# Kernel tuning notes

Hardware: AMD Instinct MI355X
Metric: run time of the kernel (lower is better)

## Reference

```python
import jax, jax.numpy as jnp
import numpy as np

NUM_EMBEDDINGS = 1024
EMBEDDING_DIM = 128
COMMITMENT_COEF = 0.25
DECAY = 0.99
EPS = 1e-5


def setup_inputs() -> dict:
    key = jax.random.key(0)
    k1, k2 = jax.random.split(key)
    z_e = jax.random.normal(k1, (64, EMBEDDING_DIM, 32, 32), dtype=jnp.float32)
    lim = 1.0 / NUM_EMBEDDINGS
    embed = jax.random.uniform(k2, (NUM_EMBEDDINGS, EMBEDDING_DIM), dtype=jnp.float32,
                               minval=-lim, maxval=lim)
    ema_cluster_size = jnp.zeros((NUM_EMBEDDINGS,), dtype=jnp.float32)
    ema_w = embed.copy()  # buffer initialized as clone of embed weights
    return {"z_e": z_e, "embed": embed,
            "ema_cluster_size": ema_cluster_size, "ema_w": ema_w}


def reference(z_e, embed, ema_cluster_size, ema_w):
    B, D, H, W = z_e.shape
    K = embed.shape[0]
    # [B,D,H,W] -> [N,D]
    flat = jnp.transpose(z_e, (0, 2, 3, 1)).reshape(-1, D)
    distances = (jnp.sum(flat ** 2, axis=1, keepdims=True)
                 + jnp.sum(embed ** 2, axis=1)
                 - 2.0 * jnp.matmul(flat, embed.T))
    encoding_indices = jnp.argmin(distances, axis=1)  # [N]

    quantized = embed[encoding_indices].reshape(B, H, W, D)
    quantized = jnp.transpose(quantized, (0, 3, 1, 2))  # [B,D,H,W]

    # ---- EMA codebook update (training path) ----
    N = flat.shape[0]
    cluster_size = jax.ops.segment_sum(jnp.ones((N,), flat.dtype),
                                       encoding_indices, num_segments=K)
    new_ema_cluster_size = DECAY * ema_cluster_size + (1.0 - DECAY) * cluster_size
    dw = jax.ops.segment_sum(flat, encoding_indices, num_segments=K)  # encodings^T @ flat
    new_ema_w = DECAY * ema_w + (1.0 - DECAY) * dw
    n = jnp.sum(new_ema_cluster_size)
    cs = (new_ema_cluster_size + EPS) / (n + K * EPS) * n
    new_embed = new_ema_w / cs[:, None]

    commitment_loss = jnp.mean((jax.lax.stop_gradient(quantized) - z_e) ** 2)
    loss = commitment_loss * COMMITMENT_COEF
    # straight-through estimator
    quantized_st = z_e + jax.lax.stop_gradient(quantized - z_e)
    indices = encoding_indices.reshape(B, H * W)
    return (quantized_st, indices, loss, new_embed, new_ema_cluster_size, new_ema_w)
```

## Files before the change

### kernel.cpp

```cpp
#include <hip/hip_runtime.h>

#define K_CODES 1024
#define DIM 128
#define HW 1024
#define NTOT 65536
#define DECAY 0.99f
#define OMD 0.01f
#define EPS 1e-5f
#define CCOEF 0.25f
#define MARGIN 1e-4f
#define FLCAP 24576

#define OFF_Q    0
#define OFF_IDX  8388608
#define OFF_LOSS (8388608 + 65536)
#define OFF_EMB  (OFF_LOSS + 1)
#define OFF_ECS  (OFF_EMB + 131072)
#define OFF_EMAW (OFF_ECS + 1024)

#define W_NORM2 0
#define W_RCP   1024
#define W_HIST  2048
#define W_LOSS  3072
#define W_FLCNT 3073
#define W_CNT2  3076
#define W_FL    (3076 + 24576)
#define W_M1F   (27652 + 24576)
#define W_CAND  (52228 + 24576)
#define W_EH    (76804 + 196608)
#define W_EL    (273412 + 65536)
#define W_NXIDX (338948 + 65536)
#define W_FLAT  (404484 + 65536)
#define W_NEED  (470020 + 8388608)

typedef __attribute__((ext_vector_type(8))) short short8v;
typedef __attribute__((ext_vector_type(4))) float f32x4;

__device__ __forceinline__ unsigned short f2bf(float f) {
    unsigned u = __float_as_uint(f);
    u += 0x7fffu + ((u >> 16) & 1u);
    return (unsigned short)(u >> 16);
}
__device__ __forceinline__ float bf2f(unsigned short h) {
    return __uint_as_float(((unsigned)h) << 16);
}

__global__ __launch_bounds__(256) void kzero(float* __restrict__ p, int n) {
    int i = blockIdx.x * 256 + threadIdx.x;
    if (i < n) p[i] = 0.f;
}

__device__ __forceinline__ float np_pairwise_sumsq_128(const float* p, size_t stride) {
    float r[8][4];
    #pragma unroll
    for (int j = 0; j < 8; ++j)
        #pragma unroll
        for (int L = 0; L < 4; ++L) {
            float x = p[(size_t)(j * 4 + L) * stride];
            r[j][L] = __fmul_rn(x, x);
        }
    #pragma unroll
    for (int c = 1; c < 4; ++c)
        #pragma unroll
        for (int j = 0; j < 8; ++j)
            #pragma unroll
            for (int L = 0; L < 4; ++L) {
                float x = p[(size_t)(c * 32 + j * 4 + L) * stride];
                r[j][L] = __fadd_rn(r[j][L], __fmul_rn(x, x));
            }
    float V[4];
    #pragma unroll
    for (int L = 0; L < 4; ++L) {
        float a = __fadd_rn(r[0][L], r[1][L]);
        float b = __fadd_rn(r[2][L], r[3][L]);
        float c2 = __fadd_rn(r[4][L], r[5][L]);
        float d2 = __fadd_rn(r[6][L], r[7][L]);
        V[L] = __fadd_rn(__fadd_rn(a, b), __fadd_rn(c2, d2));
    }
    return __fadd_rn(__fadd_rn(V[0], V[1]), __fadd_rn(V[2], V[3]));
}

__global__ __launch_bounds__(256) void kpre(
    const float* __restrict__ ze, float* __restrict__ nx,
    float* __restrict__ flat_c, const float* __restrict__ embed,
    float* __restrict__ norm2, unsigned short* __restrict__ ehs_g,
    unsigned short* __restrict__ els_g, float* __restrict__ zero_p, int zero_n)
{
    __shared__ float t[128][133];
    const int tid = threadIdx.x;
    const int bid = blockIdx.x;
    if (bid < 512) {
        const int n0 = bid * 128;
        const int b = n0 >> 10, hw0 = n0 & (HW - 1);
        const float* zb = ze + (size_t)b * (DIM * HW) + hw0;
        #pragma unroll
        for (int i = 0; i < 64; ++i) {
            int d = i * 2 + (tid >> 7);
            int hw = tid & 127;
            t[hw][d] = zb[(size_t)d * HW + hw];
        }
        __syncthreads();
        if (tid < 128) nx[n0 + tid] = np_pairwise_sumsq_128(&t[tid][0], 1);
        if (flat_c) {
            #pragma unroll
            for (int i = 0; i < 16; ++i) {
                int lin = i * 256 + tid;
                int r  = lin >> 5;
                int c4 = lin & 31;
                float4 v = *(const float4*)&t[r][c4 * 4];
                *(float4*)&flat_c[(size_t)(n0 + r) * DIM + c4 * 4] = v;
            }
        }
    } else {
        const int pid = bid - 512;
        int zi = pid * 256 + tid;
        if (zi < zero_n) zero_p[zi] = 0.f;
        {
            const int g32 = tid >> 5, l32 = tid & 31;
            const int k = pid * 8 + g32;
            const float* row = embed + (size_t)k * DIM;
            float x = row[l32];
            float r = __fmul_rn(x, x);
            #pragma unroll
            for (int c = 1; c < 4; ++c) {
                float y = row[c * 32 + l32];
                r = __fadd_rn(r, __fmul_rn(y, y));
            }
            float s1 = __fadd_rn(r, __shfl_xor(r, 4, 64));
            float s2 = __fadd_rn(s1, __shfl_xor(s1, 8, 64));
            float s3 = __fadd_rn(s2, __shfl_xor(s2, 16, 64));
            float h1 = __fadd_rn(s3, __shfl_xor(s3, 1, 64));
            float h2 = __fadd_rn(h1, __shfl_xor(h1, 2, 64));
            if (l32 == 0) norm2[k] = h2;
        }
        if (ehs_g) {
            int hu = pid * 256 + tid;
            int U = hu >> 1, half = hu & 1;
            int code = U >> 4;
            int g = (U & 15) ^ (code & 15);
            const float* src = embed + (size_t)code * DIM + g * 8 + half * 4;
            float4 f = *(const float4*)src;
            unsigned short a = f2bf(f.x), b = f2bf(f.y), c = f2bf(f.z), d = f2bf(f.w);
            ushort4 hi; hi.x = a; hi.y = b; hi.z = c; hi.w = d;
            ushort4 lo;
            lo.x = f2bf(f.x - bf2f(a)); lo.y = f2bf(f.y - bf2f(b));
            lo.z = f2bf(f.z - bf2f(c)); lo.w = f2bf(f.w - bf2f(d));
            *(ushort4*)(ehs_g + (size_t)U * 8 + half * 4) = hi;
            *(ushort4*)(els_g + (size_t)U * 8 + half * 4) = lo;
        }
    }
}

__global__ __launch_bounds__(256, 4) void kapprox(
    const float* __restrict__ flat_c, const unsigned short* __restrict__ eh_g,
    const unsigned short* __restrict__ el_g, const float* __restrict__ norm2,
    int* __restrict__ idx_ws, float* __restrict__ idx_out,
    unsigned* __restrict__ hist, unsigned* __restrict__ flcnt,
    unsigned* __restrict__ fl_list, float* __restrict__ m1f)
{
    __shared__ __align__(16) unsigned short ehs[2][32 * 128];
    __shared__ __align__(16) unsigned short els[2][32 * 128];
    __shared__ float nes[1024];

    const int tid = threadIdx.x;
    const int l = tid & 63;
    const int w = tid >> 6;
    const int lg = l >> 4;
    const int lm = l & 15;
    const int n0 = blockIdx.x * 64;

    for (int i = tid; i < 1024; i += 256) nes[i] = norm2[i];

    short8v xh[4], xl[4];
    {
        const float* xr = flat_c + (size_t)(n0 + w * 16 + lm) * DIM;
        #pragma unroll
        for (int ks = 0; ks < 4; ++ks) {
            int kb = ks * 32 + lg * 8;
            float f0[8];
            *(float4*)&f0[0] = *(const float4*)(xr + kb);
            *(float4*)&f0[4] = *(const float4*)(xr + kb + 4);
            #pragma unroll
            for (int e = 0; e < 8; ++e) {
                unsigned short h0 = f2bf(f0[e]);
                xh[ks][e] = (short)h0;
                xl[ks][e] = (short)f2bf(f0[e] - bf2f(h0));
            }
        }
    }

    int roff[4];
    #pragma unroll
    for (int ks = 0; ks < 4; ++ks)
        roff[ks] = lm * 128 + (((ks * 4 + lg) ^ lm) * 8);

    const int su0 = tid * 8;
    const int su1 = 2048 + tid * 8;

    uint4 peh0 = *(const uint4*)(eh_g + su0);
    uint4 peh1 = *(const uint4*)(eh_g + su1);
    uint4 pel0 = *(const uint4*)(el_g + su0);
    uint4 pel1 = *(const uint4*)(el_g + su1);
    *(uint4*)&ehs[0][su0] = peh0;
    *(uint4*)&ehs[0][su1] = peh1;
    *(uint4*)&els[0][su0] = pel0;
    *(uint4*)&els[0][su1] = pel1;
    __syncthreads();

    float m1 = 3.4e38f, m2 = 3.4e38f;
    int c1 = 0;

    for (int it = 0; it < 32; ++it) {
        const int buf = it & 1;
        const int nt = it + 1;
        if (nt < 32) {
            const size_t nb = (size_t)nt * 4096;
            peh0 = *(const uint4*)(eh_g + nb + su0);
            peh1 = *(const uint4*)(eh_g + nb + su1);
            pel0 = *(const uint4*)(el_g + nb + su0);
            pel1 = *(const uint4*)(el_g + nb + su1);
        }
        f32x4 a00 = {0.f,0.f,0.f,0.f}, a01 = {0.f,0.f,0.f,0.f};
        const unsigned short* be = &ehs[buf][0];
        const unsigned short* bl = &els[buf][0];
        #pragma unroll
        for (int ks = 0; ks < 4; ++ks) {
            short8v eA = *(const short8v*)(be + roff[ks]);
            short8v lA = *(const short8v*)(bl + roff[ks]);
            short8v eB = *(const short8v*)(be + 2048 + roff[ks]);
            short8v lB = *(const short8v*)(bl + 2048 + roff[ks]);
            a00 = __builtin_amdgcn_mfma_f32_16x16x32_bf16(eA, xh[ks], a00, 0, 0, 0);
            a00 = __builtin_amdgcn_mfma_f32_16x16x32_bf16(lA, xh[ks], a00, 0, 0, 0);
            a00 = __builtin_amdgcn_mfma_f32_16x16x32_bf16(eA, xl[ks], a00, 0, 0, 0);
            a01 = __builtin_amdgcn_mfma_f32_16x16x32_bf16(eB, xh[ks], a01, 0, 0, 0);
            a01 = __builtin_amdgcn_mfma_f32_16x16x32_bf16(lB, xh[ks], a01, 0, 0, 0);
            a01 = __builtin_amdgcn_mfma_f32_16x16x32_bf16(eB, xl[ks], a01, 0, 0, 0);
        }
        #pragma unroll
        for (int r = 0; r < 4; ++r) {
            int code0 = it * 32 + lg * 4 + r;
            int code1 = code0 + 16;
            float s0 = nes[code0] - 2.f * a00[r];
            float s1 = nes[code1] - 2.f * a01[r];
            m2 = fminf(m2, fmaxf(m1, s0));
            if (s0 < m1) { m1 = s0; c1 = code0; }
            m2 = fminf(m2, fmaxf(m1, s1));
            if (s1 < m1) { m1 = s1; c1 = code1; }
        }
        if (nt < 32) {
            *(uint4*)&ehs[buf ^ 1][su0] = peh0;
            *(uint4*)&ehs[buf ^ 1][su1] = peh1;
            *(uint4*)&els[buf ^ 1][su0] = pel0;
            *(uint4*)&els[buf ^ 1][su1] = pel1;
        }
        __syncthreads();
    }

    #pragma unroll
    for (int mk = 16; mk <= 32; mk <<= 1) {
        float om1 = __shfl_xor(m1, mk, 64);
        int   oc1 = __shfl_xor(c1, mk, 64);
        float om2 = __shfl_xor(m2, mk, 64);
        m2 = fminf(fminf(m2, om2), fmaxf(m1, om1));
        if (om1 < m1 || (om1 == m1 && oc1 < c1)) { m1 = om1; c1 = oc1; }
    }
    if (lg == 0) {
        int n = n0 + w * 16 + lm;
        if (m2 - m1 > MARGIN) {
            idx_ws[n] = c1;
            idx_out[n] = (float)c1;
            atomicAdd(&hist[c1], 1u);
        } else {
            unsigned p = atomicAdd(flcnt, 1u);
            if (p < FLCAP) { fl_list[p] = (unsigned)n; m1f[p] = m1; }
            else {
                idx_ws[n] = c1; idx_out[n] = (float)c1;
                atomicAdd(&hist[c1], 1u);
            }
        }
    }
}

__global__ __launch_bounds__(256, 2) void kapprox2(
    const float* __restrict__ flat_c, const unsigned short* __restrict__ eh_g,
    const unsigned short* __restrict__ el_g, const float* __restrict__ norm2,
    const float* __restrict__ m1f, const unsigned* __restrict__ flcnt,
    const unsigned* __restrict__ fl_list, unsigned* __restrict__ cnt_g,
    unsigned* __restrict__ cand_g)
{
    __shared__ __align__(16) unsigned short ehs[2][32 * 128];
    __shared__ __align__(16) unsigned short els[2][32 * 128];
    __shared__ float nes[1024];
    __shared__ unsigned ccnt[128];
    __shared__ unsigned ccode[128][8];
    __shared__ int rid[128];
    __shared__ float thrs[128];

    const int tid = threadIdx.x;
    const int l = tid & 63;
    const int w = tid >> 6;
    const int lg = l >> 4;
    const int lm = l & 15;

    for (int i = tid; i < 1024; i += 256) nes[i] = norm2[i];

    int roff[4];
    #pragma unroll
    for (int ks = 0; ks < 4; ++ks)
        roff[ks] = lm * 128 + (((ks * 4 + lg) ^ lm) * 8);

    const int su0 = tid * 8;
    const int su1 = 2048 + tid * 8;

    unsigned nflag = flcnt[0];
    if (nflag > FLCAP) nflag = FLCAP;
    const unsigned nbat = (nflag + 127u) >> 7;
    const unsigned nwork = nbat * 8u;

    for (unsigned wi = blockIdx.x; wi < nwork; wi += gridDim.x) {
        const unsigned bat = wi >> 3;
        const int cq = (int)(wi & 7u);
        __syncthreads();
        if (tid < 128) {
            unsigned p = bat * 128u + tid;
            int n = (p < nflag) ? (int)fl_list[p] : -1;
            rid[tid] = n;
            thrs[tid] = (n >= 0) ? m1f[p] + MARGIN : -3.4e38f;
            ccnt[tid] = 0;
        }
        __syncthreads();

        const int lr0 = w * 32 + lm, lr1 = lr0 + 16;
        const int nr0 = rid[lr0], nr1 = rid[lr1];
        const float thr0 = thrs[lr0], thr1 = thrs[lr1];
        short8v xh0[4], xl0[4], xh1[4], xl1[4];
        {
            const float* xr0 = flat_c + (size_t)(nr0 < 0 ? 0 : nr0) * DIM;
            const float* xr1 = flat_c + (size_t)(nr1 < 0 ? 0 : nr1) * DIM;
            #pragma unroll
            for (int ks = 0; ks < 4; ++ks) {
                int kb = ks * 32 + lg * 8;
                float f0[8], f1[8];
                *(float4*)&f0[0] = *(const float4*)(xr0 + kb);
                *(float4*)&f0[4] = *(const float4*)(xr0 + kb + 4);
                *(float4*)&f1[0] = *(const float4*)(xr1 + kb);
                *(float4*)&f1[4] = *(const float4*)(xr1 + kb + 4);
                #pragma unroll
                for (int e = 0; e < 8; ++e) {
                    unsigned short h0 = f2bf(f0[e]);
                    unsigned short h1 = f2bf(f1[e]);
                    xh0[ks][e] = (short)h0;
                    xl0[ks][e] = (short)f2bf(f0[e] - bf2f(h0));
                    xh1[ks][e] = (short)h1;
                    xl1[ks][e] = (short)f2bf(f1[e] - bf2f(h1));
                }
            }
        }

        const int it0 = cq * 4;
        uint4 peh0, peh1, pel0, pel1;
        {
            const size_t nb = (size_t)it0 * 4096;
            peh0 = *(const uint4*)(eh_g + nb + su0);
            peh1 = *(const uint4*)(eh_g + nb + su1);
            pel0 = *(const uint4*)(el_g + nb + su0);
            pel1 = *(const uint4*)(el_g + nb + su1);
            *(uint4*)&ehs[0][su0] = peh0;
            *(uint4*)&ehs[0][su1] = peh1;
            *(uint4*)&els[0][su0] = pel0;
            *(uint4*)&els[0][su1] = pel1;
        }
        __syncthreads();

        for (int ii = 0; ii < 4; ++ii) {
            const int it = it0 + ii;
            const int buf = ii & 1;
            if (ii + 1 < 4) {
                const size_t nb = (size_t)(it + 1) * 4096;
                peh0 = *(const uint4*)(eh_g + nb + su0);
                peh1 = *(const uint4*)(eh_g + nb + su1);
                pel0 = *(const uint4*)(el_g + nb + su0);
                pel1 = *(const uint4*)(el_g + nb + su1);
            }
            f32x4 a00 = {0.f,0.f,0.f,0.f}, a01 = {0.f,0.f,0.f,0.f};
            f32x4 a10 = {0.f,0.f,0.f,0.f}, a11 = {0.f,0.f,0.f,0.f};
            const unsigned short* be = &ehs[buf][0];
            const unsigned short* bl = &els[buf][0];
            #pragma unroll
            for (int ks = 0; ks < 4; ++ks) {
                short8v eA = *(const short8v*)(be + roff[ks]);
                short8v lA = *(const short8v*)(bl + roff[ks]);
                short8v eB = *(const short8v*)(be + 2048 + roff[ks]);
                short8v lB = *(const short8v*)(bl + 2048 + roff[ks]);
                a00 = __builtin_amdgcn_mfma_f32_16x16x32_bf16(eA, xh0[ks], a00, 0, 0, 0);
                a00 = __builtin_amdgcn_mfma_f32_16x16x32_bf16(lA, xh0[ks], a00, 0, 0, 0);
                a00 = __builtin_amdgcn_mfma_f32_16x16x32_bf16(eA, xl0[ks], a00, 0, 0, 0);
                a10 = __builtin_amdgcn_mfma_f32_16x16x32_bf16(eA, xh1[ks], a10, 0, 0, 0);
                a10 = __builtin_amdgcn_mfma_f32_16x16x32_bf16(lA, xh1[ks], a10, 0, 0, 0);
                a10 = __builtin_amdgcn_mfma_f32_16x16x32_bf16(eA, xl1[ks], a10, 0, 0, 0);
                a01 = __builtin_amdgcn_mfma_f32_16x16x32_bf16(eB, xh0[ks], a01, 0, 0, 0);
                a01 = __builtin_amdgcn_mfma_f32_16x16x32_bf16(lB, xh0[ks], a01, 0, 0, 0);
                a01 = __builtin_amdgcn_mfma_f32_16x16x32_bf16(eB, xl0[ks], a01, 0, 0, 0);
                a11 = __builtin_amdgcn_mfma_f32_16x16x32_bf16(eB, xh1[ks], a11, 0, 0, 0);
                a11 = __builtin_amdgcn_mfma_f32_16x16x32_bf16(lB, xh1[ks], a11, 0, 0, 0);
                a11 = __builtin_amdgcn_mfma_f32_16x16x32_bf16(eB, xl1[ks], a11, 0, 0, 0);
            }
            #pragma unroll
            for (int r = 0; r < 4; ++r) {
                int code0 = it * 32 + lg * 4 + r;
                int code1 = code0 + 16;
                float s00 = nes[code0] - 2.f * a00[r];
                float s01 = nes[code1] - 2.f * a01[r];
                float s10 = nes[code0] - 2.f * a10[r];
                float s11 = nes[code1] - 2.f * a11[r];
                if (s00 <= thr0) {
                    unsigned p = atomicAdd(&ccnt[lr0], 1u);
                    if (p < 8) ccode[lr0][p] = (unsigned)code0;
                }
                if (s01 <= thr0) {
                    unsigned p = atomicAdd(&ccnt[lr0], 1u);
                    if (p < 8) ccode[lr0][p] = (unsigned)code1;
                }
                if (s10 <= thr1) {
                    unsigned p = atomicAdd(&ccnt[lr1], 1u);
                    if (p < 8) ccode[lr1][p] = (unsigned)code0;
                }
                if (s11 <= thr1) {
                    unsigned p = atomicAdd(&ccnt[lr1], 1u);
                    if (p < 8) ccode[lr1][p] = (unsigned)code1;
                }
            }
            if (ii + 1 < 4) {
                *(uint4*)&ehs[buf ^ 1][su0] = peh0;
                *(uint4*)&ehs[buf ^ 1][su1] = peh1;
                *(uint4*)&els[buf ^ 1][su0] = pel0;
                *(uint4*)&els[buf ^ 1][su1] = pel1;
            }
            __syncthreads();
        }

        if (tid < 128) {
            int n = rid[tid];
            unsigned lc = ccnt[tid];
            if (lc > 8u) lc = 8u;
            if (n >= 0 && lc > 0) {
                unsigned p = bat * 128u + tid;
                unsigned base = atomicAdd(&cnt_g[p], lc);
                for (unsigned j = 0; j < lc; ++j) {
                    unsigned slot = base + j;
                    if (slot < 8u) cand_g[(size_t)p * 8 + slot] = ccode[tid][j];
                }
            }
        }
    }
}

__global__ __launch_bounds__(256) void krescore(
    const float* __restrict__ flat_c, const float* __restrict__ embed,
    const float* __restrict__ norm2, const float* nxg,
    const unsigned* __restrict__ flcnt, const unsigned* __restrict__ fl_list,
    const unsigned* __restrict__ cnt_g, const unsigned* __restrict__ cand_g,
    int* idx_ws, float* __restrict__ idx_out, unsigned* __restrict__ hist)
{
    unsigned nflag = flcnt[0];
    if (nflag > FLCAP) nflag = FLCAP;
    for (unsigned p = blockIdx.x * 256u + threadIdx.x; p < nflag;
         p += gridDim.x * 256u) {
        const int n = (int)fl_list[p];
        unsigned c = cnt_g[p];
        if (c > 8u) c = 8u;
        unsigned cc[8];
        uint4 pk0 = *(const uint4*)(cand_g + (size_t)p * 8);
        uint4 pk1 = *(const uint4*)(cand_g + (size_t)p * 8 + 4);
        cc[0] = pk0.x; cc[1] = pk0.y; cc[2] = pk0.z; cc[3] = pk0.w;
        cc[4] = pk1.x; cc[5] = pk1.y; cc[6] = pk1.z; cc[7] = pk1.w;
        int bestk = (int)cc[0];
        if (c > 1) {
            float bests = 3.4e38f;
            bestk = 1 << 30;
            const float* xr = flat_c + (size_t)n * DIM;
            const float nx = nxg[n];
            #pragma unroll
            for (int q = 0; q < 8; ++q) {
                if (q < (int)c) {
                    int k = (int)cc[q];
                    const float* er = embed + (size_t)k * DIM;
                    float dot = 0.f;
                    #pragma unroll
                    for (int d4 = 0; d4 < 32; ++d4) {
                        float4 e4 = *(const float4*)(er + d4 * 4);
                        float4 x4 = *(const float4*)(xr + d4 * 4);
                        dot = fmaf(x4.x, e4.x, dot);
                        dot = fmaf(x4.y, e4.y, dot);
                        dot = fmaf(x4.z, e4.z, dot);
                        dot = fmaf(x4.w, e4.w, dot);
                    }
                    float qv = __fadd_rn(nx, norm2[k]);
                    float s = __fsub_rn(qv, __fmul_rn(2.f, dot));
                    if (s < bests || (s == bests && k < bestk)) { bests = s; bestk = k; }
                }
            }
        }
        idx_ws[n] = bestk;
        idx_out[n] = (float)bestk;
        atomicAdd(&hist[bestk], 1u);
    }
}

__global__ __launch_bounds__(256) void kfin_r(
    const unsigned int* __restrict__ hist, const float* __restrict__ ema_cs,
    float* __restrict__ out_ecs, float* __restrict__ rcp)
{
    const int tid = threadIdx.x;
    __shared__ float wsum[4];
    float local = 0.f;
    float necs[4];
    #pragma unroll
    for (int u = 0; u < 4; ++u) {
        int k = u * 256 + tid;
        necs[u] = DECAY * ema_cs[k] + OMD * (float)hist[k];
        out_ecs[k] = necs[u];
        local += necs[u];
    }
    #pragma unroll
    for (int off = 32; off >= 1; off >>= 1) local += __shfl_xor(local, off, 64);
    if ((tid & 63) == 0) wsum[tid >> 6] = local;
    __syncthreads();
    float ntot = wsum[0] + wsum[1] + wsum[2] + wsum[3];
    #pragma unroll
    for (int u = 0; u < 4; ++u) {
        int k = u * 256 + tid;
        float cs = (necs[u] + EPS) / (ntot + (float)K_CODES * EPS) * ntot;
        rcp[k] = 1.f / cs;
    }
}

__global__ __launch_bounds__(64) void kloss(
    float* __restrict__ loss_out, const float* __restrict__ loss_acc)
{
    if (threadIdx.x == 0)
        loss_out[0] = loss_acc[0] * (CCOEF / (float)((size_t)NTOT * DIM));
}

__global__ __launch_bounds__(512) void ktail(
    const float* __restrict__ ze, const float* __restrict__ embed,
    const int* __restrict__ idx_ws, float* __restrict__ qout,
    float* __restrict__ loss_acc, const float* __restrict__ flat_c,
    const float* __restrict__ ema_w, const float* __restrict__ rcp,
    float* __restrict__ out_emb, float* __restrict__ out_emaw)
{
    __shared__ float shmem[64 * 133];
    __shared__ int idxs[64];
    __shared__ float lsum[8];
    const int tid = threadIdx.x;
    const int bid = blockIdx.x;
    if (bid < 1024) {
        const int n0 = bid * 64;
        const int b = n0 >> 10;
        const int hw0 = n0 & (HW - 1);
        if (tid < 64) idxs[tid] = idx_ws[n0 + tid];
        __syncthreads();
        #pragma unroll
        for (int it = 0; it < 4; ++it) {
            int lin = it * 512 + tid;
            int r = lin >> 5, c4 = lin & 31;
            float4 v = *(const float4*)(embed + (size_t)idxs[r] * DIM + c4 * 4);
            *(float4*)&shmem[r * 133 + c4 * 4] = v;
        }
        __syncthreads();
        const float* zb = ze + (size_t)b * (DIM * HW) + hw0;
        float* qb = qout + (size_t)b * (DIM * HW) + hw0;
        const int hwl = tid & 63;
        float lacc = 0.f;
        #pragma unroll 4
        for (int dd = 0; dd < 16; ++dd) {
            int d = dd * 8 + (tid >> 6);
            float val = shmem[hwl * 133 + d];
            size_t off = (size_t)d * HW + hwl;
            float z = zb[off];
            qb[off] = val;
            float diff = val - z;
            lacc = fmaf(diff, diff, lacc);
        }
        #pragma unroll
        for (int off = 32; off >= 1; off >>= 1) lacc += __shfl_xor(lacc, off, 64);
        if ((tid & 63) == 0) lsum[tid >> 6] = lacc;
        __syncthreads();
        if (tid == 0) {
            float s = ((lsum[0] + lsum[1]) + (lsum[2] + lsum[3]))
                    + ((lsum[4] + lsum[5]) + (lsum[6] + lsum[7]));
            atomicAdd(loss_acc, s);
        }
    } else {
        float (*part)[128] = (float(*)[128])shmem;
        const int k = bid - 1024;
        const int lane = tid & 63;
        const int w = tid >> 6;
        float lo = 0.f, hi = 0.f;
        const int nbeg = w * (NTOT / 8);
        const int nend = nbeg + (NTOT / 8);
        for (int base = nbeg; base < nend; base += 64) {
            int my = idx_ws[base + lane];
            unsigned long long m = __ballot(my == k);
            while (m) {
                int bit = __ffsll((long long)m) - 1;
                m &= m - 1;
                const float* row = flat_c + (size_t)(base + bit) * DIM;
                lo += row[lane];
                hi += row[lane + 64];
            }
        }
        part[w][lane] = lo;
        part[w][lane + 64] = hi;
        __syncthreads();
        if (w == 0) {
            float a = part[0][lane], bsum = part[0][lane + 64];
            #pragma unroll
            for (int u = 1; u < 8; ++u) {
                a += part[u][lane];
                bsum += part[u][lane + 64];
            }
            const float r = rcp[k];
            int elo = k * DIM + lane, ehi = elo + 64;
            float nwa = DECAY * ema_w[elo] + OMD * a;
            float nwb = DECAY * ema_w[ehi] + OMD * bsum;
            out_emaw[elo] = nwa;
            out_emaw[ehi] = nwb;
            out_emb[elo] = nwa * r;
            out_emb[ehi] = nwb * r;
        }
    }
}

__global__ __launch_bounds__(256, 2) void kargmin(
    const float* __restrict__ ze, const float* __restrict__ embed,
    const float* __restrict__ norm2, const float* nxg,
    int* idx_ws, float* __restrict__ idx_out,
    unsigned int* __restrict__ hist)
{
    __shared__ float xs[128 * 36];
    __shared__ float es[128 * 36];
    __shared__ float nxs[128];
    const int tid = threadIdx.x;
    const int tx = tid & 15, ty = tid >> 4;
    const int n0 = blockIdx.x * 128;
    const float* zbase = ze + (size_t)(n0 >> 10) * (DIM * HW) + (n0 & (HW - 1));
    if (tid < 128) nxs[tid] = nxg[n0 + tid];
    float minv[8];
    int   mini[8];
    #pragma unroll
    for (int i = 0; i < 8; ++i) { minv[i] = 3.4e38f; mini[i] = 0; }
    for (int kt = 0; kt < 8; ++kt) {
        float acc[8][8];
        #pragma unroll
        for (int i = 0; i < 8; ++i)
            #pragma unroll
            for (int j = 0; j < 8; ++j) acc[i][j] = 0.f;
        for (int dc = 0; dc < 4; ++dc) {
            __syncthreads();
            #pragma unroll
            for (int it = 0; it < 4; ++it) {
                int lin = it * 256 + tid;
                int r  = lin & 127;
                int gu = lin >> 7;
                const float* gp = zbase + (size_t)(dc * 32 + gu * 4) * HW + r;
                float4 v;
                v.x = gp[0]; v.y = gp[HW]; v.z = gp[2 * HW]; v.w = gp[3 * HW];
                *(float4*)&xs[r * 36 + gu * 4] = v;
            }
            #pragma unroll
            for (int it = 0; it < 4; ++it) {
                int lin = it * 256 + tid;
                int k  = lin >> 3;
                int gu = lin & 7;
                float4 v = *(const float4*)(embed + (size_t)(kt * 128 + k) * DIM + dc * 32 + gu * 4);
                *(float4*)&es[k * 36 + gu * 4] = v;
            }
            __syncthreads();
            #pragma unroll
            for (int g = 0; g < 8; ++g) {
                float4 xf[8];
                #pragma unroll
                for (int i = 0; i < 8; ++i)
                    xf[i] = *(const float4*)&xs[(ty + i * 16) * 36 + g * 4];
                #pragma unroll
                for (int j = 0; j < 8; ++j) {
                    float4 ef = *(const float4*)&es[(tx + j * 16) * 36 + g * 4];
                    #pragma unroll
                    for (int i = 0; i < 8; ++i) {
                        acc[i][j] = fmaf(xf[i].x, ef.x, acc[i][j]);
                        acc[i][j] = fmaf(xf[i].y, ef.y, acc[i][j]);
                        acc[i][j] = fmaf(xf[i].z, ef.z, acc[i][j]);
                        acc[i][j] = fmaf(xf[i].w, ef.w, acc[i][j]);
                    }
                }
            }
        }
        #pragma unroll
        for (int j = 0; j < 8; ++j) {
            int kg = kt * 128 + tx + j * 16;
            float nrm = norm2[kg];
            #pragma unroll
            for (int i = 0; i < 8; ++i) {
                float q = __fadd_rn(nxs[ty + i * 16], nrm);
                float t = __fmul_rn(2.f, acc[i][j]);
                float s = __fsub_rn(q, t);
                if (s < minv[i]) { minv[i] = s; mini[i] = kg; }
            }
        }
    }
    #pragma unroll
    for (int i = 0; i < 8; ++i) {
        float v = minv[i]; int ix = mini[i];
        #pragma unroll
        for (int off = 8; off >= 1; off >>= 1) {
            float v2 = __shfl_xor(v, off, 16);
            int   i2 = __shfl_xor(ix, off, 16);
            if (v2 < v || (v2 == v && i2 < ix)) { v = v2; ix = i2; }
        }
        if (tx == 0) {
            int n = n0 + ty + i * 16;
            idx_ws[n] = ix;
            idx_out[n] = (float)ix;
            atomicAdd(&hist[ix], 1u);
        }
    }
}

__global__ __launch_bounds__(256) void kquant(
    const float* __restrict__ ze, const float* __restrict__ embed,
    const int* __restrict__ idx_ws, float* __restrict__ qout,
    float* __restrict__ dw_atomic, float* __restrict__ loss_acc)
{
    __shared__ float q[128 * 133];
    __shared__ int idxs[128];
    __shared__ float lsum[4];
    const int tid = threadIdx.x;
    const int n0 = blockIdx.x * 128;
    const int b = n0 >> 10;
    const int hw0 = n0 & (HW - 1);
    if (tid < 128) idxs[tid] = idx_ws[n0 + tid];
    __syncthreads();
    #pragma unroll
    for (int it = 0; it < 16; ++it) {
        int r = it * 8 + (tid >> 5);
        int c = tid & 31;
        float4 v = *(const float4*)(embed + (size_t)idxs[r] * DIM + c * 4);
        *(float4*)&q[r * 133 + c * 4] = v;
    }
    __syncthreads();
    const float* zb = ze + (size_t)b * (DIM * HW) + hw0;
    float* qb = qout + (size_t)b * (DIM * HW) + hw0;
    float lacc = 0.f;
    for (int dd = 0; dd < 64; ++dd) {
        int d = dd * 2 + (tid >> 7);
        int hw = tid & 127;
        float val = q[hw * 133 + d];
        size_t off = (size_t)d * HW + hw;
        float z = zb[off];
        qb[off] = val;
        float diff = val - z;
        lacc = fmaf(diff, diff, lacc);
        if (dw_atomic) atomicAdd(&dw_atomic[idxs[hw] * DIM + d], z);
    }
    #pragma unroll
    for (int off = 32; off >= 1; off >>= 1) lacc += __shfl_xor(lacc, off, 64);
    if ((tid & 63) == 0) lsum[tid >> 6] = lacc;
    __syncthreads();
    if (tid == 0) atomicAdd(loss_acc, lsum[0] + lsum[1] + lsum[2] + lsum[3]);
}

__global__ __launch_bounds__(256) void kfin1(
    const unsigned int* __restrict__ hist, const float* __restrict__ ema_cs,
    float* __restrict__ out_ecs, float* __restrict__ rcp,
    float* __restrict__ loss_out, const float* __restrict__ loss_acc)
{
    const int tid = threadIdx.x;
    __shared__ float wsum[4];
    float local = 0.f;
    float necs[4];
    #pragma unroll
    for (int u = 0; u < 4; ++u) {
        int k = u * 256 + tid;
        necs[u] = DECAY * ema_cs[k] + OMD * (float)hist[k];
        out_ecs[k] = necs[u];
        local += necs[u];
    }
    #pragma unroll
    for (int off = 32; off >= 1; off >>= 1) local += __shfl_xor(local, off, 64);
    if ((tid & 63) == 0) wsum[tid >> 6] = local;
    __syncthreads();
    float ntot = wsum[0] + wsum[1] + wsum[2] + wsum[3];
    #pragma unroll
    for (int u = 0; u < 4; ++u) {
        int k = u * 256 + tid;
        float cs = (necs[u] + EPS) / (ntot + (float)K_CODES * EPS) * ntot;
        rcp[k] = 1.f / cs;
    }
    if (tid == 0) loss_out[0] = loss_acc[0] * (CCOEF / (float)((size_t)NTOT * DIM));
}

__global__ __launch_bounds__(256) void kfin2(
    const float* __restrict__ ema_w, const float* __restrict__ dw,
    const float* __restrict__ rcp, float* __restrict__ out_emb,
    float* __restrict__ out_emaw)
{
    int e = blockIdx.x * 256 + threadIdx.x;
    int k = e >> 7;
    float nw = DECAY * ema_w[e] + OMD * dw[e];
    out_emaw[e] = nw;
    out_emb[e] = nw * rcp[k];
}

extern "C" void kernel_launch(void* const* d_in, const int* in_sizes, int n_in,
                              void* d_out, int out_size, void* d_ws, size_t ws_size,
                              hipStream_t stream) {
    const float* ze     = (const float*)d_in[0];
    const float* embed  = (const float*)d_in[1];
    const float* ema_cs = (const float*)d_in[2];
    const float* ema_w  = (const float*)d_in[3];
    float* out = (float*)d_out;

    float* ws = (float*)d_ws;
    float*          ws_norm2 = ws + W_NORM2;
    float*          ws_rcp   = ws + W_RCP;
    unsigned*       ws_hist  = (unsigned*)(ws + W_HIST);
    float*          ws_loss  = ws + W_LOSS;
    unsigned*       ws_flcnt = (unsigned*)(ws + W_FLCNT);
    unsigned*       ws_cnt   = (unsigned*)(ws + W_CNT2);
    unsigned*       ws_fl    = (unsigned*)(ws + W_FL);
    float*          ws_m1    = ws + W_M1F;
    unsigned*       ws_cand  = (unsigned*)(ws + W_CAND);
    float*          ws_dw    = ws + W_CAND;
    unsigned short* ws_eh    = (unsigned short*)(ws + W_EH);
    unsigned short* ws_el    = (unsigned short*)(ws + W_EL);
    float*          ws_nx    = ws + W_NXIDX;
    int*            ws_idx   = (int*)(ws + W_NXIDX);
    float*          ws_flat  = ws + W_FLAT;
    const size_t need = (size_t)W_NEED * sizeof(float);
    const bool big_ws = ws_size >= need;

    if (big_ws) {
        hipLaunchKernelGGL(kpre, dim3(640), dim3(256), 0, stream,
                           ze, ws_nx, ws_flat, embed, ws_norm2, ws_eh, ws_el,
                           (float*)ws_hist, 25604);
        hipLaunchKernelGGL(kapprox, dim3(1024), dim3(256), 0, stream,
                           ws_flat, ws_eh, ws_el, ws_norm2,
                           ws_idx, out + OFF_IDX, ws_hist, ws_flcnt, ws_fl, ws_m1);
        hipLaunchKernelGGL(kapprox2, dim3(512), dim3(256), 0, stream,
                           ws_flat, ws_eh, ws_el, ws_norm2,
                           ws_m1, ws_flcnt, ws_fl, ws_cnt, ws_cand);
        hipLaunchKernelGGL(krescore, dim3(64), dim3(256), 0, stream,
                           ws_flat, embed, ws_norm2, ws_nx, ws_flcnt, ws_fl,
                           ws_cnt, ws_cand, ws_idx, out + OFF_IDX, ws_hist);
        hipLaunchKernelGGL(kfin_r, dim3(1), dim3(256), 0, stream,
                           ws_hist, ema_cs, out + OFF_ECS, ws_rcp);
        hipLaunchKernelGGL(ktail, dim3(2048), dim3(512), 0, stream,
                           ze, embed, ws_idx, out + OFF_Q, ws_loss,
                           ws_flat, ema_w, ws_rcp, out + OFF_EMB, out + OFF_EMAW);
        hipLaunchKernelGGL(kloss, dim3(1), dim3(64), 0, stream,
                           out + OFF_LOSS, ws_loss);
    } else {
        hipLaunchKernelGGL(kpre, dim3(640), dim3(256), 0, stream,
                           ze, ws_nx, (float*)nullptr, embed, ws_norm2,
                           (unsigned short*)nullptr, (unsigned short*)nullptr,
                           (float*)ws_hist, 1028);
        hipLaunchKernelGGL(kzero, dim3(512), dim3(256), 0, stream, ws_dw, 131072);
        hipLaunchKernelGGL(kargmin, dim3(512), dim3(256), 0, stream,
                           ze, embed, ws_norm2, ws_nx, ws_idx, out + OFF_IDX, ws_hist);
        hipLaunchKernelGGL(kquant, dim3(512), dim3(256), 0, stream,
                           ze, embed, ws_idx, out + OFF_Q, ws_dw, ws_loss);
        hipLaunchKernelGGL(kfin1, dim3(1), dim3(256), 0, stream,
                           ws_hist, ema_cs, out + OFF_ECS, ws_rcp, out + OFF_LOSS, ws_loss);
        hipLaunchKernelGGL(kfin2, dim3(512), dim3(256), 0, stream,
                           ema_w, ws_dw, ws_rcp, out + OFF_EMB, out + OFF_EMAW);
    }
}
```

Measured before the change: 170.3 us.

## Fold finalize and loss kernels into predecessors via last-block atomic counters

```diff
diff --git a/kernel.cpp b/kernel.cpp
--- a/kernel.cpp
+++ b/kernel.cpp
@@ -23,6 +23,8 @@
 #define W_HIST  2048
 #define W_LOSS  3072
 #define W_FLCNT 3073
+#define W_RDONE 3074
+#define W_QDONE 3075
 #define W_CNT2  3076
 #define W_FL    (3076 + 24576)
 #define W_M1F   (27652 + 24576)
@@ -207,8 +209,8 @@
     *(uint4*)&els[0][su1] = pel1;
     __syncthreads();
 
-    float m1 = 3.4e38f, m2 = 3.4e38f;
-    int c1 = 0;
+    float m1a = 3.4e38f, m2a = 3.4e38f, m1b = 3.4e38f, m2b = 3.4e38f;
+    int c1a = 0, c1b = 0;
 
     for (int it = 0; it < 32; ++it) {
         const int buf = it & 1;
@@ -242,10 +244,10 @@
             int code1 = code0 + 16;
             float s0 = nes[code0] - 2.f * a00[r];
             float s1 = nes[code1] - 2.f * a01[r];
-            m2 = fminf(m2, fmaxf(m1, s0));
-            if (s0 < m1) { m1 = s0; c1 = code0; }
-            m2 = fminf(m2, fmaxf(m1, s1));
-            if (s1 < m1) { m1 = s1; c1 = code1; }
+            m2a = fminf(m2a, fmaxf(m1a, s0));
+            if (s0 < m1a) { m1a = s0; c1a = code0; }
+            m2b = fminf(m2b, fmaxf(m1b, s1));
+            if (s1 < m1b) { m1b = s1; c1b = code1; }
         }
         if (nt < 32) {
             *(uint4*)&ehs[buf ^ 1][su0] = peh0;
@@ -255,6 +257,10 @@
         }
         __syncthreads();
     }
+
+    float m1 = m1a, m2 = fminf(fminf(m2a, m2b), fmaxf(m1a, m1b));
+    int c1 = c1a;
+    if (m1b < m1a || (m1b == m1a && c1b < c1a)) { m1 = m1b; c1 = c1b; }
 
     #pragma unroll
     for (int mk = 16; mk <= 32; mk <<= 1) {
@@ -460,7 +466,9 @@
     const float* __restrict__ norm2, const float* nxg,
     const unsigned* __restrict__ flcnt, const unsigned* __restrict__ fl_list,
     const unsigned* __restrict__ cnt_g, const unsigned* __restrict__ cand_g,
-    int* idx_ws, float* __restrict__ idx_out, unsigned* __restrict__ hist)
+    int* idx_ws, float* __restrict__ idx_out, unsigned* hist,
+    unsigned* __restrict__ rdone, const float* __restrict__ ema_cs,
+    float* __restrict__ out_ecs, float* __restrict__ rcp)
 {
     unsigned nflag = flcnt[0];
     if (nflag > FLCAP) nflag = FLCAP;
@@ -505,49 +513,44 @@
         idx_out[n] = (float)bestk;
         atomicAdd(&hist[bestk], 1u);
     }
-}
-
-__global__ __launch_bounds__(256) void kfin_r(
-    const unsigned int* __restrict__ hist, const float* __restrict__ ema_cs,
-    float* __restrict__ out_ecs, float* __restrict__ rcp)
-{
-    const int tid = threadIdx.x;
-    __shared__ float wsum[4];
-    float local = 0.f;
-    float necs[4];
-    #pragma unroll
-    for (int u = 0; u < 4; ++u) {
-        int k = u * 256 + tid;
-        necs[u] = DECAY * ema_cs[k] + OMD * (float)hist[k];
-        out_ecs[k] = necs[u];
-        local += necs[u];
-    }
-    #pragma unroll
-    for (int off = 32; off >= 1; off >>= 1) local += __shfl_xor(local, off, 64);
-    if ((tid & 63) == 0) wsum[tid >> 6] = local;
+    __shared__ unsigned lastv;
+    __threadfence();
+    if (threadIdx.x == 0) lastv = atomicAdd(rdone, 1u);
     __syncthreads();
-    float ntot = wsum[0] + wsum[1] + wsum[2] + wsum[3];
-    #pragma unroll
-    for (int u = 0; u < 4; ++u) {
-        int k = u * 256 + tid;
-        float cs = (necs[u] + EPS) / (ntot + (float)K_CODES * EPS) * ntot;
-        rcp[k] = 1.f / cs;
-    }
-}
-
-__global__ __launch_bounds__(64) void kloss(
-    float* __restrict__ loss_out, const float* __restrict__ loss_acc)
-{
-    if (threadIdx.x == 0)
-        loss_out[0] = loss_acc[0] * (CCOEF / (float)((size_t)NTOT * DIM));
+    if (lastv == gridDim.x - 1) {
+        const int tid = threadIdx.x;
+        __shared__ float wsum[4];
+        float local = 0.f;
+        float necs[4];
+        #pragma unroll
+        for (int u = 0; u < 4; ++u) {
+            int k = u * 256 + tid;
+            unsigned h = atomicAdd(&hist[k], 0u);
+            necs[u] = DECAY * ema_cs[k] + OMD * (float)h;
+            out_ecs[k] = necs[u];
+            local += necs[u];
+        }
+        #pragma unroll
+        for (int off = 32; off >= 1; off >>= 1) local += __shfl_xor(local, off, 64);
+        if ((tid & 63) == 0) wsum[tid >> 6] = local;
+        __syncthreads();
+        float ntot = wsum[0] + wsum[1] + wsum[2] + wsum[3];
+        #pragma unroll
+        for (int u = 0; u < 4; ++u) {
+            int k = u * 256 + tid;
+            float cs = (necs[u] + EPS) / (ntot + (float)K_CODES * EPS) * ntot;
+            rcp[k] = 1.f / cs;
+        }
+    }
 }
 
 __global__ __launch_bounds__(512) void ktail(
     const float* __restrict__ ze, const float* __restrict__ embed,
     const int* __restrict__ idx_ws, float* __restrict__ qout,
-    float* __restrict__ loss_acc, const float* __restrict__ flat_c,
+    float* loss_acc, const float* __restrict__ flat_c,
     const float* __restrict__ ema_w, const float* __restrict__ rcp,
-    float* __restrict__ out_emb, float* __restrict__ out_emaw)
+    float* __restrict__ out_emb, float* __restrict__ out_emaw,
+    unsigned* __restrict__ qdone, float* __restrict__ loss_out)
 {
     __shared__ float shmem[64 * 133];
     __shared__ int idxs[64];
@@ -590,6 +593,12 @@
             float s = ((lsum[0] + lsum[1]) + (lsum[2] + lsum[3]))
                     + ((lsum[4] + lsum[5]) + (lsum[6] + lsum[7]));
             atomicAdd(loss_acc, s);
+            __threadfence();
+            unsigned old = atomicAdd(qdone, 1u);
+            if (old == 1023u) {
+                float tot = atomicAdd(loss_acc, 0.f);
+                loss_out[0] = tot * (CCOEF / (float)((size_t)NTOT * DIM));
+            }
         }
     } else {
         float (*part)[128] = (float(*)[128])shmem;
@@ -827,6 +836,8 @@
     unsigned*       ws_hist  = (unsigned*)(ws + W_HIST);
     float*          ws_loss  = ws + W_LOSS;
     unsigned*       ws_flcnt = (unsigned*)(ws + W_FLCNT);
+    unsigned*       ws_rdone = (unsigned*)(ws + W_RDONE);
+    unsigned*       ws_qdone = (unsigned*)(ws + W_QDONE);
     unsigned*       ws_cnt   = (unsigned*)(ws + W_CNT2);
     unsigned*       ws_fl    = (unsigned*)(ws + W_FL);
     float*          ws_m1    = ws + W_M1F;
@@ -852,14 +863,12 @@
                            ws_m1, ws_flcnt, ws_fl, ws_cnt, ws_cand);
         hipLaunchKernelGGL(krescore, dim3(64), dim3(256), 0, stream,
                            ws_flat, embed, ws_norm2, ws_nx, ws_flcnt, ws_fl,
-                           ws_cnt, ws_cand, ws_idx, out + OFF_IDX, ws_hist);
-        hipLaunchKernelGGL(kfin_r, dim3(1), dim3(256), 0, stream,
-                           ws_hist, ema_cs, out + OFF_ECS, ws_rcp);
+                           ws_cnt, ws_cand, ws_idx, out + OFF_IDX, ws_hist,
+                           ws_rdone, ema_cs, out + OFF_ECS, ws_rcp);
         hipLaunchKernelGGL(ktail, dim3(2048), dim3(512), 0, stream,
                            ze, embed, ws_idx, out + OFF_Q, ws_loss,
-                           ws_flat, ema_w, ws_rcp, out + OFF_EMB, out + OFF_EMAW);
-        hipLaunchKernelGGL(kloss, dim3(1), dim3(64), 0, stream,
-                           out + OFF_LOSS, ws_loss);
+                           ws_flat, ema_w, ws_rcp, out + OFF_EMB, out + OFF_EMAW,
+                           ws_qdone, out + OFF_LOSS);
     } else {
         hipLaunchKernelGGL(kpre, dim3(640), dim3(256), 0, stream,
                            ze, ws_nx, (float*)nullptr, embed, ws_norm2,
```

Measured after the change: 200.8 us. 1.18x slower.

## Switch kapprox to 32x32x16 MFMA with 32 rows per wave

Applied to the files above, without the earlier changes.

```diff
diff --git a/kernel.cpp b/kernel.cpp
--- a/kernel.cpp
+++ b/kernel.cpp
@@ -35,6 +35,7 @@
 
 typedef __attribute__((ext_vector_type(8))) short short8v;
 typedef __attribute__((ext_vector_type(4))) float f32x4;
+typedef __attribute__((ext_vector_type(16))) float f32x16;
 
 __device__ __forceinline__ unsigned short f2bf(float f) {
     unsigned u = __float_as_uint(f);
@@ -151,7 +152,7 @@
     }
 }
 
-__global__ __launch_bounds__(256, 4) void kapprox(
+__global__ __launch_bounds__(256, 2) void kapprox(
     const float* __restrict__ flat_c, const unsigned short* __restrict__ eh_g,
     const unsigned short* __restrict__ el_g, const float* __restrict__ norm2,
     int* __restrict__ idx_ws, float* __restrict__ idx_out,
@@ -165,18 +166,18 @@
     const int tid = threadIdx.x;
     const int l = tid & 63;
     const int w = tid >> 6;
-    const int lg = l >> 4;
-    const int lm = l & 15;
-    const int n0 = blockIdx.x * 64;
+    const int hi = l >> 5;
+    const int ln = l & 31;
+    const int n0 = blockIdx.x * 128;
 
     for (int i = tid; i < 1024; i += 256) nes[i] = norm2[i];
 
-    short8v xh[4], xl[4];
+    short8v xh[8], xl[8];
     {
-        const float* xr = flat_c + (size_t)(n0 + w * 16 + lm) * DIM;
-        #pragma unroll
-        for (int ks = 0; ks < 4; ++ks) {
-            int kb = ks * 32 + lg * 8;
+        const float* xr = flat_c + (size_t)(n0 + w * 32 + ln) * DIM;
+        #pragma unroll
+        for (int ks = 0; ks < 8; ++ks) {
+            int kb = ks * 16 + hi * 8;
             float f0[8];
             *(float4*)&f0[0] = *(const float4*)(xr + kb);
             *(float4*)&f0[4] = *(const float4*)(xr + kb + 4);
@@ -189,10 +190,10 @@
         }
     }
 
-    int roff[4];
-    #pragma unroll
-    for (int ks = 0; ks < 4; ++ks)
-        roff[ks] = lm * 128 + (((ks * 4 + lg) ^ lm) * 8);
+    int roff[8];
+    #pragma unroll
+    for (int ks = 0; ks < 8; ++ks)
+        roff[ks] = ln * 128 + ((((ks * 2) + hi) ^ (l & 15)) * 8);
 
     const int su0 = tid * 8;
     const int su1 = 2048 + tid * 8;
@@ -220,32 +221,26 @@
             pel0 = *(const uint4*)(el_g + nb + su0);
             pel1 = *(const uint4*)(el_g + nb + su1);
         }
-        f32x4 a00 = {0.f,0.f,0.f,0.f}, a01 = {0.f,0.f,0.f,0.f};
+        f32x16 accA = {0.f,0.f,0.f,0.f,0.f,0.f,0.f,0.f,
+                       0.f,0.f,0.f,0.f,0.f,0.f,0.f,0.f};
+        f32x16 accB = accA;
         const unsigned short* be = &ehs[buf][0];
         const unsigned short* bl = &els[buf][0];
         #pragma unroll
-        for (int ks = 0; ks < 4; ++ks) {
-            short8v eA = *(const short8v*)(be + roff[ks]);
-            short8v lA = *(const short8v*)(bl + roff[ks]);
-            short8v eB = *(const short8v*)(be + 2048 + roff[ks]);
-            short8v lB = *(const short8v*)(bl + 2048 + roff[ks]);
-            a00 = __builtin_amdgcn_mfma_f32_16x16x32_bf16(eA, xh[ks], a00, 0, 0, 0);
-            a00 = __builtin_amdgcn_mfma_f32_16x16x32_bf16(lA, xh[ks], a00, 0, 0, 0);
-            a00 = __builtin_amdgcn_mfma_f32_16x16x32_bf16(eA, xl[ks], a00, 0, 0, 0);
-            a01 = __builtin_amdgcn_mfma_f32_16x16x32_bf16(eB, xh[ks], a01, 0, 0, 0);
-            a01 = __builtin_amdgcn_mfma_f32_16x16x32_bf16(lB, xh[ks], a01, 0, 0, 0);
-            a01 = __builtin_amdgcn_mfma_f32_16x16x32_bf16(eB, xl[ks], a01, 0, 0, 0);
-        }
-        #pragma unroll
-        for (int r = 0; r < 4; ++r) {
-            int code0 = it * 32 + lg * 4 + r;
-            int code1 = code0 + 16;
-            float s0 = nes[code0] - 2.f * a00[r];
-            float s1 = nes[code1] - 2.f * a01[r];
-            m2 = fminf(m2, fmaxf(m1, s0));
-            if (s0 < m1) { m1 = s0; c1 = code0; }
-            m2 = fminf(m2, fmaxf(m1, s1));
-            if (s1 < m1) { m1 = s1; c1 = code1; }
+        for (int ks = 0; ks < 8; ++ks) {
+            short8v eh8 = *(const short8v*)(be + roff[ks]);
+            short8v el8 = *(const short8v*)(bl + roff[ks]);
+            accA = __builtin_amdgcn_mfma_f32_32x32x16_bf16(eh8, xh[ks], accA, 0, 0, 0);
+            accA = __builtin_amdgcn_mfma_f32_32x32x16_bf16(el8, xh[ks], accA, 0, 0, 0);
+            accB = __builtin_amdgcn_mfma_f32_32x32x16_bf16(eh8, xl[ks], accB, 0, 0, 0);
+        }
+        #pragma unroll
+        for (int r = 0; r < 16; ++r) {
+            int code = it * 32 + (r & 3) + 8 * (r >> 2) + 4 * hi;
+            float a = accA[r] + accB[r];
+            float s = nes[code] - 2.f * a;
+            m2 = fminf(m2, fmaxf(m1, s));
+            if (s < m1) { m1 = s; c1 = code; }
         }
         if (nt < 32) {
             *(uint4*)&ehs[buf ^ 1][su0] = peh0;
@@ -256,16 +251,15 @@
         __syncthreads();
     }
 
-    #pragma unroll
-    for (int mk = 16; mk <= 32; mk <<= 1) {
-        float om1 = __shfl_xor(m1, mk, 64);
-        int   oc1 = __shfl_xor(c1, mk, 64);
-        float om2 = __shfl_xor(m2, mk, 64);
+    {
+        float om1 = __shfl_xor(m1, 32, 64);
+        int   oc1 = __shfl_xor(c1, 32, 64);
+        float om2 = __shfl_xor(m2, 32, 64);
         m2 = fminf(fminf(m2, om2), fmaxf(m1, om1));
         if (om1 < m1 || (om1 == m1 && oc1 < c1)) { m1 = om1; c1 = oc1; }
     }
-    if (lg == 0) {
-        int n = n0 + w * 16 + lm;
+    if (hi == 0) {
+        int n = n0 + w * 32 + ln;
         if (m2 - m1 > MARGIN) {
             idx_ws[n] = c1;
             idx_out[n] = (float)c1;
@@ -844,7 +838,7 @@
         hipLaunchKernelGGL(kpre, dim3(640), dim3(256), 0, stream,
                            ze, ws_nx, ws_flat, embed, ws_norm2, ws_eh, ws_el,
                            (float*)ws_hist, 25604);
-        hipLaunchKernelGGL(kapprox, dim3(1024), dim3(256), 0, stream,
+        hipLaunchKernelGGL(kapprox, dim3(512), dim3(256), 0, stream,
                            ws_flat, ws_eh, ws_el, ws_norm2,
                            ws_idx, out + OFF_IDX, ws_hist, ws_flcnt, ws_fl, ws_m1);
         hipLaunchKernelGGL(kapprox2, dim3(512), dim3(256), 0, stream,
```

Measured after the change: 172.4 us. No clear change (+1.2%).
